# Optimization experiments

Measured on AMD Instinct MI355X. Metric: run time of the kernel, lower is better.

## Reference

```python
import jax, jax.numpy as jnp
import numpy as np

N = 50000   # nodes
E = 640000  # edges per outer layer
D = 128     # in_channels == num_hidden_channels
H = 4       # attention heads
C = D // H  # per-head dim = 32
BS = 1024   # batch_size for output slice
LN_EPS = 1e-12


def setup_inputs() -> dict:
    key = jax.random.key(0)
    ks = jax.random.split(key, 16)
    w = lambda k, shape: (jax.random.normal(k, shape, dtype=jnp.float32) * 0.05)
    return {
        "embs": jax.random.normal(ks[0], (N, D), dtype=jnp.float32),
        # GATv2 conv 0 (shared lin_l == lin_r since share_weights=True)
        "w0": w(ks[1], (D, H * C)),
        "b0": w(ks[2], (H * C,)),
        "att0": w(ks[3], (H, C)),
        "bias0": w(ks[4], (H * C,)),
        # GATv2 conv 1
        "w1": w(ks[5], (D, H * C)),
        "b1": w(ks[6], (H * C,)),
        "att1": w(ks[7], (H, C)),
        "bias1": w(ks[8], (H * C,)),
        # output head: Linear(D, D) + LayerNorm(D)
        "wout": w(ks[9], (D, D)),
        "bout": w(ks[10], (D,)),
        "gamma": jnp.ones((D,), dtype=jnp.float32),
        "beta": jnp.zeros((D,), dtype=jnp.float32),
        # graph structure (row 0 = source j, row 1 = target i, PyG convention)
        "edge_index0": jax.random.randint(ks[11], (2, E), 0, N, dtype=jnp.int32),
        "edge_index1": jax.random.randint(ks[12], (2, E), 0, N, dtype=jnp.int32),
        "batch_size": BS,
    }


def gatv2_conv(x, edge_index, w, b, att, bias):
    """PyG GATv2Conv: share_weights=True, add_self_loops=False, concat=True,
    negative_slope=0.2, edge_attr=None, eval mode (no attention dropout)."""
    xl = (x @ w + b).reshape(-1, H, C)          # [N, H, C]; x_l == x_r
    src, dst = edge_index[0], edge_index[1]
    xj = xl[src]                                # messages  [E, H, C]
    e = jax.nn.leaky_relu(xl[dst] + xj, negative_slope=0.2)
    alpha = jnp.einsum("ehc,hc->eh", e, att)    # [E, H]
    # segment softmax over incoming edges of each target node
    amax = jax.ops.segment_max(alpha, dst, num_segments=N)
    alpha = jnp.exp(alpha - amax[dst])
    denom = jax.ops.segment_sum(alpha, dst, num_segments=N)
    alpha = alpha / denom[dst]
    out = jax.ops.segment_sum(alpha[:, :, None] * xj, dst, num_segments=N)
    return out.reshape(-1, H * C) + bias        # [N, H*C]


def reference(embs, w0, b0, att0, bias0, w1, b1, att1, bias1,
              wout, bout, gamma, beta, edge_index0, edge_index1, batch_size):
    x = gatv2_conv(embs, edge_index0, w0, b0, att0, bias0)
    x = jax.nn.gelu(x, approximate=False)       # nn.GELU default (dropout is eval no-op)
    x = gatv2_conv(x, edge_index1, w1, b1, att1, bias1)
    # layernorm_output head on first batch_size nodes
    y = x[:batch_size] @ wout + bout
    mu = jnp.mean(y, axis=-1, keepdims=True)
    var = jnp.mean(jnp.square(y - mu), axis=-1, keepdims=True)
    return (y - mu) * jax.lax.rsqrt(var + LN_EPS) * gamma + beta
```

## Files before the change

kernel.cpp:

```cpp
#include <hip/hip_runtime.h>
#include <math.h>

#define DD 128
#define SLOT 64

typedef short bf16x8 __attribute__((ext_vector_type(8)));
typedef float f32x4  __attribute__((ext_vector_type(4)));

__device__ __forceinline__ unsigned bf16rne(float f) {
    unsigned u = __float_as_uint(f);
    return (u + 0x7FFFu + ((u >> 16) & 1u)) >> 16;
}
__device__ __forceinline__ float2 bf2f(unsigned u) {
    float2 r;
    r.x = __uint_as_float(u << 16);
    r.y = __uint_as_float(u & 0xFFFF0000u);
    return r;
}
__device__ __forceinline__ float gelu1(float v) {
    return 0.5f * v * (1.f + erff(v * 0.70710678118654752f));
}

__global__ __launch_bounds__(256) void k_zero(int* __restrict__ p, int T) {
    int stride = gridDim.x * 256;
    for (int i = blockIdx.x * 256 + threadIdx.x; i < T; i += stride) p[i] = 0;
}

__global__ __launch_bounds__(256) void k_mark(const int* __restrict__ src1,
                                              const int* __restrict__ dst1,
                                              int E1, int BS,
                                              unsigned* __restrict__ mb,
                                              int* __restrict__ livelist,
                                              int* __restrict__ nLive,
                                              int* __restrict__ cnt,
                                              int* __restrict__ ssrc, int N,
                                              const float* __restrict__ w0,
                                              const float* __restrict__ w1,
                                              unsigned short* __restrict__ wp0,
                                              unsigned short* __restrict__ wp1) {
    __shared__ int lbuf[1280];
    __shared__ int lcnt, lbase;
    if (threadIdx.x == 0) lcnt = 0;
    __syncthreads();

    int idx = blockIdx.x * 256 + threadIdx.x;
    if (idx < 2 * DD * DD) {
        const float* w = (idx < DD * DD) ? w0 : w1;
        unsigned short* wp = (idx < DD * DD) ? wp0 : wp1;
        int i = idx & (DD * DD - 1);
        int k = i >> 7, c = i & 127;
        int nt = c >> 4, ks = k >> 5;
        int lane = (c & 15) | (((k >> 3) & 3) << 4);
        wp[(((nt * 4 + ks) * 64) + lane) * 8 + (k & 7)] =
            (unsigned short)bf16rne(w[k * DD + c]);
    }

    int base = blockIdx.x * 1024 + threadIdx.x;
    #pragma unroll
    for (int j = 0; j < 4; ++j) {
        int e = base + j * 256;
        if (e < E1) {
            int d = dst1[e];
            if (d < BS) {
                int s = src1[e];
                int r = atomicAdd(&cnt[N + d], 1);
                if (r < SLOT) ssrc[(size_t)(N + d) * SLOT + r] = s;
                unsigned old = atomicOr(&mb[s >> 5], 1u << (s & 31));
                if (!((old >> (s & 31)) & 1u))
                    lbuf[atomicAdd(&lcnt, 1)] = s;
            }
        }
    }
    int g = blockIdx.x * 256 + threadIdx.x;
    if (g < BS) {
        unsigned old = atomicOr(&mb[g >> 5], 1u << (g & 31));
        if (!((old >> (g & 31)) & 1u))
            lbuf[atomicAdd(&lcnt, 1)] = g;
    }
    __syncthreads();
    if (threadIdx.x == 0) lbase = atomicAdd(nLive, lcnt);
    __syncthreads();
    for (int i = threadIdx.x; i < lcnt; i += 256) livelist[lbase + i] = lbuf[i];
}

__global__ __launch_bounds__(256) void k_hflin(
        const float* __restrict__ x, const unsigned short* __restrict__ wp,
        const float* __restrict__ b, unsigned* __restrict__ y, int nrows,
        int gLin,
        const int* __restrict__ src0, const int* __restrict__ dst0, int E0,
        const unsigned* __restrict__ mb, int* __restrict__ cnt,
        int* __restrict__ ssrc) {
    __shared__ bf16x8 wl[2048];

    if (blockIdx.x >= gLin) {
        int role = blockIdx.x - gLin;
        int base = role * 1024 + threadIdx.x;
        #pragma unroll
        for (int j = 0; j < 4; ++j) {
            int e = base + j * 256;
            if (e < E0) {
                int d = dst0[e];
                if ((mb[d >> 5] >> (d & 31)) & 1u) {
                    int r = atomicAdd(&cnt[d], 1);
                    if (r < SLOT) ssrc[(size_t)d * SLOT + r] = src0[e];
                }
            }
        }
        return;
    }

    const bf16x8* wg = (const bf16x8*)wp;
    #pragma unroll
    for (int i = 0; i < 8; ++i)
        wl[threadIdx.x + i * 256] = wg[threadIdx.x + i * 256];
    __syncthreads();

    int wave = threadIdx.x >> 6;
    int rb = blockIdx.x * 64 + wave * 16;
    int lane = threadIdx.x & 63;
    int c = lane & 15, g = lane >> 4;
    int rIn = rb + c;
    int rowValid = rIn < nrows;

    f32x4 acc[8];
    #pragma unroll
    for (int nt = 0; nt < 8; ++nt) {
        float bb = b[nt * 16 + c];
        acc[nt] = (f32x4){bb, bb, bb, bb};
    }
    for (int ks = 0; ks < 4; ++ks) {
        float xr[8];
        if (rowValid) {
            const float4* xp = (const float4*)&x[(size_t)rIn * DD + ks * 32 + g * 8];
            *(float4*)&xr[0] = xp[0];
            *(float4*)&xr[4] = xp[1];
        } else {
            #pragma unroll
            for (int j = 0; j < 8; ++j) xr[j] = 0.f;
        }
        union { unsigned u[4]; bf16x8 v; } af;
        #pragma unroll
        for (int j = 0; j < 4; ++j)
            af.u[j] = bf16rne(xr[2 * j]) | (bf16rne(xr[2 * j + 1]) << 16);
        #pragma unroll
        for (int nt = 0; nt < 8; ++nt) {
            bf16x8 bv = wl[(nt * 4 + ks) * 64 + lane];
            acc[nt] = __builtin_amdgcn_mfma_f32_16x16x32_bf16(af.v, bv, acc[nt], 0, 0, 0);
        }
    }
    int g4 = g * 4;
    #pragma unroll
    for (int nt = 0; nt < 8; ++nt) {
        #pragma unroll
        for (int reg = 0; reg < 4; ++reg) {
            unsigned u = bf16rne(acc[nt][reg]);
            unsigned up = (unsigned)__shfl_xor((int)u, 1, 64);
            int row = rb + g4 + reg;
            if (!(c & 1) && row < nrows)
                y[(size_t)row * 64 + (nt * 16 + c) / 2] = u | (up << 16);
        }
    }
}

__global__ __launch_bounds__(256) void k_aggL(const unsigned* __restrict__ xl,
                                              const int* __restrict__ cnt,
                                              const int* __restrict__ ssrc,
                                              const float* __restrict__ att,
                                              const float* __restrict__ bias,
                                              float* __restrict__ out,
                                              const int* __restrict__ livelist,
                                              const int* __restrict__ nLive) {
    int li = blockIdx.x * 4 + (threadIdx.x >> 6);
    if (li >= *nLive) return;
    int node = __builtin_amdgcn_readfirstlane(livelist[li]);
    int lane = threadIdx.x & 63;
    float2 attv = *(const float2*)&att[lane * 2];
    float2 xd = bf2f(xl[(size_t)node * 64 + lane]);
    int rs  = node * SLOT;
    int deg = cnt[node];
    deg = deg > SLOT ? SLOT : deg;

    float m = -3.4e38f, den = 0.f, accx = 0.f, accy = 0.f;
    int sA = (deg > 0) ? ssrc[rs] : 0;
    int sB = (deg > 1) ? ssrc[rs + 1] : 0;
    unsigned uA = xl[(size_t)sA * 64 + lane];
    unsigned uB = xl[(size_t)sB * 64 + lane];

    int k = 0;
    for (; k + 1 < deg; k += 2) {
        int sC = (k + 2 < deg) ? ssrc[rs + k + 2] : 0;
        int sD = (k + 3 < deg) ? ssrc[rs + k + 3] : 0;
        unsigned uC = xl[(size_t)sC * 64 + lane];
        unsigned uD = xl[(size_t)sD * 64 + lane];
        float2 vA = bf2f(uA), vB = bf2f(uB);

        float tx = xd.x + vA.x, ty = xd.y + vA.y;
        tx = tx > 0.f ? tx : 0.2f * tx;
        ty = ty > 0.f ? ty : 0.2f * ty;
        float l0 = tx * attv.x + ty * attv.y;
        tx = xd.x + vB.x; ty = xd.y + vB.y;
        tx = tx > 0.f ? tx : 0.2f * tx;
        ty = ty > 0.f ? ty : 0.2f * ty;
        float l1 = tx * attv.x + ty * attv.y;
        #pragma unroll
        for (int o = 8; o; o >>= 1) {
            l0 += __shfl_xor(l0, o, 64);
            l1 += __shfl_xor(l1, o, 64);
        }
        float mn = fmaxf(fmaxf(m, l0), l1);
        float corr = __expf(m - mn);
        float w0 = __expf(l0 - mn);
        float w1 = __expf(l1 - mn);
        den  = den  * corr + w0 + w1;
        accx = accx * corr + w0 * vA.x + w1 * vB.x;
        accy = accy * corr + w0 * vA.y + w1 * vB.y;
        m = mn;
        sA = sC; sB = sD; uA = uC; uB = uD;
    }
    if (k < deg) {
        float2 vA = bf2f(uA);
        float tx = xd.x + vA.x, ty = xd.y + vA.y;
        tx = tx > 0.f ? tx : 0.2f * tx;
        ty = ty > 0.f ? ty : 0.2f * ty;
        float l0 = tx * attv.x + ty * attv.y;
        #pragma unroll
        for (int o = 8; o; o >>= 1) l0 += __shfl_xor(l0, o, 64);
        float mn = fmaxf(m, l0);
        float corr = __expf(m - mn);
        float w0 = __expf(l0 - mn);
        den  = den  * corr + w0;
        accx = accx * corr + w0 * vA.x;
        accy = accy * corr + w0 * vA.y;
    }

    float inv = (deg > 0) ? 1.f / den : 0.f;
    float2 o2;
    o2.x = accx * inv + bias[lane * 2];
    o2.y = accy * inv + bias[lane * 2 + 1];
    *(float2*)&out[(size_t)node * DD + lane * 2] = o2;
}

__global__ __launch_bounds__(256) void k_linC(const float* __restrict__ x,
                                              const unsigned short* __restrict__ wp,
                                              const float* __restrict__ b,
                                              unsigned* __restrict__ y,
                                              const int* __restrict__ livelist,
                                              const int* __restrict__ nLive) {
    __shared__ bf16x8 wl[2048];
    int nL = *nLive;
    if (blockIdx.x * 64 >= nL) return;

    const bf16x8* wg = (const bf16x8*)wp;
    #pragma unroll
    for (int i = 0; i < 8; ++i)
        wl[threadIdx.x + i * 256] = wg[threadIdx.x + i * 256];
    __syncthreads();

    int wave = threadIdx.x >> 6;
    int lb = blockIdx.x * 64 + wave * 16;
    int lane = threadIdx.x & 63;
    int c = lane & 15, g = lane >> 4;
    int liIn = lb + c;
    int rIn = (liIn < nL) ? livelist[liIn] : 0;

    f32x4 acc[8];
    #pragma unroll
    for (int nt = 0; nt < 8; ++nt) {
        float bb = b[nt * 16 + c];
        acc[nt] = (f32x4){bb, bb, bb, bb};
    }
    for (int ks = 0; ks < 4; ++ks) {
        float xr[8];
        if (liIn < nL) {
            const float4* xp = (const float4*)&x[(size_t)rIn * DD + ks * 32 + g * 8];
            *(float4*)&xr[0] = xp[0];
            *(float4*)&xr[4] = xp[1];
            #pragma unroll
            for (int j = 0; j < 8; ++j) xr[j] = gelu1(xr[j]);
        } else {
            #pragma unroll
            for (int j = 0; j < 8; ++j) xr[j] = 0.f;
        }
        union { unsigned u[4]; bf16x8 v; } af;
        #pragma unroll
        for (int j = 0; j < 4; ++j)
            af.u[j] = bf16rne(xr[2 * j]) | (bf16rne(xr[2 * j + 1]) << 16);
        #pragma unroll
        for (int nt = 0; nt < 8; ++nt) {
            bf16x8 bv = wl[(nt * 4 + ks) * 64 + lane];
            acc[nt] = __builtin_amdgcn_mfma_f32_16x16x32_bf16(af.v, bv, acc[nt], 0, 0, 0);
        }
    }
    int g4 = g * 4;
    #pragma unroll
    for (int reg = 0; reg < 4; ++reg) {
        int liOut = lb + g4 + reg;
        int row = (liOut < nL) ? livelist[liOut] : -1;
        #pragma unroll
        for (int nt = 0; nt < 8; ++nt) {
            unsigned u = bf16rne(acc[nt][reg]);
            unsigned up = (unsigned)__shfl_xor((int)u, 1, 64);
            if (!(c & 1) && row >= 0)
                y[(size_t)row * 64 + (nt * 16 + c) / 2] = u | (up << 16);
        }
    }
}

__global__ __launch_bounds__(256) void k_agg1head(
        const unsigned* __restrict__ xl,
        const int* __restrict__ cnt, const int* __restrict__ ssrc,
        const float* __restrict__ att, const float* __restrict__ bias,
        const float* __restrict__ wout, const float* __restrict__ bout,
        const float* __restrict__ gamma, const float* __restrict__ beta,
        float* __restrict__ yout, int N, int BS) {
    __shared__ float xrow[4][DD];
    int wid  = threadIdx.x >> 6;
    int lane = threadIdx.x & 63;
    int node = blockIdx.x * 4 + wid;
    if (node >= BS) return;
    float2 attv = *(const float2*)&att[lane * 2];
    float2 xd = bf2f(xl[(size_t)node * 64 + lane]);
    int key = N + node;
    int rs  = key * SLOT;
    int deg = cnt[key];
    deg = deg > SLOT ? SLOT : deg;

    float m = -3.4e38f, den = 0.f, accx = 0.f, accy = 0.f;
    int sA = (deg > 0) ? ssrc[rs] : 0;
    int sB = (deg > 1) ? ssrc[rs + 1] : 0;
    unsigned uA = xl[(size_t)sA * 64 + lane];
    unsigned uB = xl[(size_t)sB * 64 + lane];

    int k = 0;
    for (; k + 1 < deg; k += 2) {
        int sC = (k + 2 < deg) ? ssrc[rs + k + 2] : 0;
        int sD = (k + 3 < deg) ? ssrc[rs + k + 3] : 0;
        unsigned uC = xl[(size_t)sC * 64 + lane];
        unsigned uD = xl[(size_t)sD * 64 + lane];
        float2 vA = bf2f(uA), vB = bf2f(uB);
        float tx = xd.x + vA.x, ty = xd.y + vA.y;
        tx = tx > 0.f ? tx : 0.2f * tx;
        ty = ty > 0.f ? ty : 0.2f * ty;
        float l0 = tx * attv.x + ty * attv.y;
        tx = xd.x + vB.x; ty = xd.y + vB.y;
        tx = tx > 0.f ? tx : 0.2f * tx;
        ty = ty > 0.f ? ty : 0.2f * ty;
        float l1 = tx * attv.x + ty * attv.y;
        #pragma unroll
        for (int o = 8; o; o >>= 1) {
            l0 += __shfl_xor(l0, o, 64);
            l1 += __shfl_xor(l1, o, 64);
        }
        float mn = fmaxf(fmaxf(m, l0), l1);
        float corr = __expf(m - mn);
        float w0 = __expf(l0 - mn);
        float w1 = __expf(l1 - mn);
        den  = den  * corr + w0 + w1;
        accx = accx * corr + w0 * vA.x + w1 * vB.x;
        accy = accy * corr + w0 * vA.y + w1 * vB.y;
        m = mn;
        sA = sC; sB = sD; uA = uC; uB = uD;
    }
    if (k < deg) {
        float2 vA = bf2f(uA);
        float tx = xd.x + vA.x, ty = xd.y + vA.y;
        tx = tx > 0.f ? tx : 0.2f * tx;
        ty = ty > 0.f ? ty : 0.2f * ty;
        float l0 = tx * attv.x + ty * attv.y;
        #pragma unroll
        for (int o = 8; o; o >>= 1) l0 += __shfl_xor(l0, o, 64);
        float mn = fmaxf(m, l0);
        float corr = __expf(m - mn);
        float w0 = __expf(l0 - mn);
        den  = den  * corr + w0;
        accx = accx * corr + w0 * vA.x;
        accy = accy * corr + w0 * vA.y;
    }

    float inv = (deg > 0) ? 1.f / den : 0.f;
    float2 o2;
    o2.x = accx * inv + bias[lane * 2];
    o2.y = accy * inv + bias[lane * 2 + 1];

    xrow[wid][lane * 2]     = o2.x;
    xrow[wid][lane * 2 + 1] = o2.y;
    float2 acc2 = *(const float2*)&bout[lane * 2];
    __syncthreads();
    #pragma unroll 4
    for (int kk = 0; kk < DD; ++kk) {
        float xv = xrow[wid][kk];
        float2 wv2 = *(const float2*)&wout[(size_t)kk * DD + lane * 2];
        acc2.x += xv * wv2.x;
        acc2.y += xv * wv2.y;
    }
    float s = acc2.x + acc2.y;
    #pragma unroll
    for (int o = 32; o; o >>= 1) s += __shfl_xor(s, o, 64);
    float mean = s * (1.f / 128.f);
    float dx = acc2.x - mean, dy = acc2.y - mean;
    float s2 = dx * dx + dy * dy;
    #pragma unroll
    for (int o = 32; o; o >>= 1) s2 += __shfl_xor(s2, o, 64);
    float rstd = rsqrtf(s2 * (1.f / 128.f) + 1e-12f);
    float2 g2 = *(const float2*)&gamma[lane * 2];
    float2 b2 = *(const float2*)&beta[lane * 2];
    float2 yo;
    yo.x = dx * rstd * g2.x + b2.x;
    yo.y = dy * rstd * g2.y + b2.y;
    *(float2*)&yout[(size_t)node * DD + lane * 2] = yo;
}

extern "C" void kernel_launch(void* const* d_in, const int* in_sizes, int n_in,
                              void* d_out, int out_size, void* d_ws, size_t ws_size,
                              hipStream_t stream) {
    const float* embs  = (const float*)d_in[0];
    const float* w0    = (const float*)d_in[1];
    const float* b0    = (const float*)d_in[2];
    const float* att0  = (const float*)d_in[3];
    const float* bias0 = (const float*)d_in[4];
    const float* w1    = (const float*)d_in[5];
    const float* b1    = (const float*)d_in[6];
    const float* att1  = (const float*)d_in[7];
    const float* bias1 = (const float*)d_in[8];
    const float* wout  = (const float*)d_in[9];
    const float* bout  = (const float*)d_in[10];
    const float* gamma = (const float*)d_in[11];
    const float* beta  = (const float*)d_in[12];
    const int* ei0 = (const int*)d_in[13];
    const int* ei1 = (const int*)d_in[14];

    int N  = in_sizes[0] / DD;
    int E0 = in_sizes[13] / 2;
    int E1 = in_sizes[14] / 2;
    int BS = out_size / DD;
    int n2 = N + BS;
    int W  = (N + 31) / 32;

    unsigned* xl   = (unsigned*)d_ws;
    float* out     = (float*)(xl + (size_t)N * 64);
    int* ssrc      = (int*)(out + (size_t)N * DD);
    int* cnt       = ssrc + (size_t)n2 * SLOT;
    unsigned* mb   = (unsigned*)(cnt + n2);
    int* nLive     = (int*)(mb + W + 32);
    int* livelist  = nLive + 1;
    unsigned short* wp0 = (unsigned short*)
        (((uintptr_t)(livelist + N) + 15) & ~(uintptr_t)15);
    unsigned short* wp1 = wp0 + DD * DD;

    int gH0  = (E0 + 1023) / 1024;
    int gH1  = (E1 + 1023) / 1024;
    int gLin = (N + 63) / 64;
    int Tz   = n2 + W + 32 + 1;

    k_zero<<<64, 256, 0, stream>>>(cnt, Tz);
    k_mark<<<gH1, 256, 0, stream>>>(ei1, ei1 + E1, E1, BS, mb, livelist, nLive,
                                    cnt, ssrc, N, w0, w1, wp0, wp1);
    k_hflin<<<gLin + gH0, 256, 0, stream>>>(
        embs, wp0, b0, xl, N, gLin, ei0, ei0 + E0, E0, mb, cnt, ssrc);
    k_aggL<<<(N + 3) / 4, 256, 0, stream>>>(xl, cnt, ssrc, att0, bias0, out,
                                            livelist, nLive);
    k_linC<<<gLin, 256, 0, stream>>>(out, wp1, b1, xl, livelist, nLive);
    k_agg1head<<<(BS + 3) / 4, 256, 0, stream>>>(
        xl, cnt, ssrc, att1, bias1,
        wout, bout, gamma, beta, (float*)d_out, N, BS);
}
```

Measured before the change: 79.74 us.

## Fuse GELU and bf16 packing into layer-0 aggregation; overlap count zeroing with marking

The layer-0 aggregation now applies bias, GELU and bf16 packing before storing, so the intermediate buffer shrinks from fp32 to packed bf16. The second linear kernel then loads bf16 fragments directly and drops its GELU and conversion work. Zeroing of the first-layer count array moves into extra blocks of the marking kernel, leaving a much smaller standalone zero kernel. The risk is a race: those zeroing blocks run concurrently with marking, which only touches the cnt[N+d] half, so this looks safe but depends on block ordering for nothing else.

```diff
diff --git a/kernel.cpp b/kernel.cpp
--- a/kernel.cpp
+++ b/kernel.cpp
@@ -21,7 +21,7 @@
     return 0.5f * v * (1.f + erff(v * 0.70710678118654752f));
 }
 
-__global__ __launch_bounds__(256) void k_zero(int* __restrict__ p, int T) {
+__global__ __launch_bounds__(256) void k_zero2(int* __restrict__ p, int T) {
     int stride = gridDim.x * 256;
     for (int i = blockIdx.x * 256 + threadIdx.x; i < T; i += stride) p[i] = 0;
 }
@@ -37,13 +37,21 @@
                                               const float* __restrict__ w0,
                                               const float* __restrict__ w1,
                                               unsigned short* __restrict__ wp0,
-                                              unsigned short* __restrict__ wp1) {
+                                              unsigned short* __restrict__ wp1,
+                                              int gZ) {
+    if (blockIdx.x < gZ) {
+        int stride = gZ * 256;
+        for (int i = blockIdx.x * 256 + threadIdx.x; i < N; i += stride)
+            cnt[i] = 0;
+        return;
+    }
     __shared__ int lbuf[1280];
     __shared__ int lcnt, lbase;
     if (threadIdx.x == 0) lcnt = 0;
     __syncthreads();
 
-    int idx = blockIdx.x * 256 + threadIdx.x;
+    int role = blockIdx.x - gZ;
+    int idx = role * 256 + threadIdx.x;
     if (idx < 2 * DD * DD) {
         const float* w = (idx < DD * DD) ? w0 : w1;
         unsigned short* wp = (idx < DD * DD) ? wp0 : wp1;
@@ -55,7 +63,7 @@
             (unsigned short)bf16rne(w[k * DD + c]);
     }
 
-    int base = blockIdx.x * 1024 + threadIdx.x;
+    int base = role * 1024 + threadIdx.x;
     #pragma unroll
     for (int j = 0; j < 4; ++j) {
         int e = base + j * 256;
@@ -71,7 +79,7 @@
             }
         }
     }
-    int g = blockIdx.x * 256 + threadIdx.x;
+    int g = role * 256 + threadIdx.x;
     if (g < BS) {
         unsigned old = atomicOr(&mb[g >> 5], 1u << (g & 31));
         if (!((old >> (g & 31)) & 1u))
@@ -143,10 +151,9 @@
         for (int j = 0; j < 4; ++j)
             af.u[j] = bf16rne(xr[2 * j]) | (bf16rne(xr[2 * j + 1]) << 16);
         #pragma unroll
-        for (int nt = 0; nt < 8; ++nt) {
-            bf16x8 bv = wl[(nt * 4 + ks) * 64 + lane];
-            acc[nt] = __builtin_amdgcn_mfma_f32_16x16x32_bf16(af.v, bv, acc[nt], 0, 0, 0);
-        }
+        for (int nt = 0; nt < 8; ++nt)
+            acc[nt] = __builtin_amdgcn_mfma_f32_16x16x32_bf16(
+                af.v, wl[(nt * 4 + ks) * 64 + lane], acc[nt], 0, 0, 0);
     }
     int g4 = g * 4;
     #pragma unroll
@@ -167,7 +174,7 @@
                                               const int* __restrict__ ssrc,
                                               const float* __restrict__ att,
                                               const float* __restrict__ bias,
-                                              float* __restrict__ out,
+                                              unsigned* __restrict__ xg,
                                               const int* __restrict__ livelist,
                                               const int* __restrict__ nLive) {
     int li = blockIdx.x * 4 + (threadIdx.x >> 6);
@@ -234,13 +241,12 @@
     }
 
     float inv = (deg > 0) ? 1.f / den : 0.f;
-    float2 o2;
-    o2.x = accx * inv + bias[lane * 2];
-    o2.y = accy * inv + bias[lane * 2 + 1];
-    *(float2*)&out[(size_t)node * DD + lane * 2] = o2;
-}
-
-__global__ __launch_bounds__(256) void k_linC(const float* __restrict__ x,
+    float gx = gelu1(accx * inv + bias[lane * 2]);
+    float gy = gelu1(accy * inv + bias[lane * 2 + 1]);
+    xg[(size_t)node * 64 + lane] = bf16rne(gx) | (bf16rne(gy) << 16);
+}
+
+__global__ __launch_bounds__(256) void k_linC(const unsigned* __restrict__ xg,
                                               const unsigned short* __restrict__ wp,
                                               const float* __restrict__ b,
                                               unsigned* __restrict__ y,
@@ -262,6 +268,7 @@
     int c = lane & 15, g = lane >> 4;
     int liIn = lb + c;
     int rIn = (liIn < nL) ? livelist[liIn] : 0;
+    const uint4* xp = (const uint4*)&xg[(size_t)rIn * 64];
 
     f32x4 acc[8];
     #pragma unroll
@@ -269,27 +276,15 @@
         float bb = b[nt * 16 + c];
         acc[nt] = (f32x4){bb, bb, bb, bb};
     }
+    #pragma unroll
     for (int ks = 0; ks < 4; ++ks) {
-        float xr[8];
-        if (liIn < nL) {
-            const float4* xp = (const float4*)&x[(size_t)rIn * DD + ks * 32 + g * 8];
-            *(float4*)&xr[0] = xp[0];
-            *(float4*)&xr[4] = xp[1];
-            #pragma unroll
-            for (int j = 0; j < 8; ++j) xr[j] = gelu1(xr[j]);
-        } else {
-            #pragma unroll
-            for (int j = 0; j < 8; ++j) xr[j] = 0.f;
-        }
-        union { unsigned u[4]; bf16x8 v; } af;
-        #pragma unroll
-        for (int j = 0; j < 4; ++j)
-            af.u[j] = bf16rne(xr[2 * j]) | (bf16rne(xr[2 * j + 1]) << 16);
-        #pragma unroll
-        for (int nt = 0; nt < 8; ++nt) {
-            bf16x8 bv = wl[(nt * 4 + ks) * 64 + lane];
-            acc[nt] = __builtin_amdgcn_mfma_f32_16x16x32_bf16(af.v, bv, acc[nt], 0, 0, 0);
-        }
+        union { uint4 q; bf16x8 v; } af;
+        if (liIn < nL) af.q = xp[ks * 4 + g];
+        else           af.q = make_uint4(0, 0, 0, 0);
+        #pragma unroll
+        for (int nt = 0; nt < 8; ++nt)
+            acc[nt] = __builtin_amdgcn_mfma_f32_16x16x32_bf16(
+                af.v, wl[(nt * 4 + ks) * 64 + lane], acc[nt], 0, 0, 0);
     }
     int g4 = g * 4;
     #pragma unroll
@@ -437,8 +432,8 @@
     int W  = (N + 31) / 32;
 
     unsigned* xl   = (unsigned*)d_ws;
-    float* out     = (float*)(xl + (size_t)N * 64);
-    int* ssrc      = (int*)(out + (size_t)N * DD);
+    unsigned* xg   = xl + (size_t)N * 64;
+    int* ssrc      = (int*)(xg + (size_t)N * 64);
     int* cnt       = ssrc + (size_t)n2 * SLOT;
     unsigned* mb   = (unsigned*)(cnt + n2);
     int* nLive     = (int*)(mb + W + 32);
@@ -450,16 +445,18 @@
     int gH0  = (E0 + 1023) / 1024;
     int gH1  = (E1 + 1023) / 1024;
     int gLin = (N + 63) / 64;
-    int Tz   = n2 + W + 32 + 1;
-
-    k_zero<<<64, 256, 0, stream>>>(cnt, Tz);
-    k_mark<<<gH1, 256, 0, stream>>>(ei1, ei1 + E1, E1, BS, mb, livelist, nLive,
-                                    cnt, ssrc, N, w0, w1, wp0, wp1);
+    int gZ   = 48;
+    int Tz2  = BS + W + 32 + 1;
+
+    k_zero2<<<4, 256, 0, stream>>>(cnt + N, Tz2);
+    k_mark<<<gZ + gH1, 256, 0, stream>>>(ei1, ei1 + E1, E1, BS, mb, livelist,
+                                         nLive, cnt, ssrc, N, w0, w1, wp0, wp1,
+                                         gZ);
     k_hflin<<<gLin + gH0, 256, 0, stream>>>(
         embs, wp0, b0, xl, N, gLin, ei0, ei0 + E0, E0, mb, cnt, ssrc);
-    k_aggL<<<(N + 3) / 4, 256, 0, stream>>>(xl, cnt, ssrc, att0, bias0, out,
+    k_aggL<<<(N + 3) / 4, 256, 0, stream>>>(xl, cnt, ssrc, att0, bias0, xg,
                                             livelist, nLive);
-    k_linC<<<gLin, 256, 0, stream>>>(out, wp1, b1, xl, livelist, nLive);
+    k_linC<<<gLin, 256, 0, stream>>>(xg, wp1, b1, xl, livelist, nLive);
     k_agg1head<<<(BS + 3) / 4, 256, 0, stream>>>(
         xl, cnt, ssrc, att1, bias1,
         wout, bout, gamma, beta, (float*)d_out, N, BS);
```

Result: faster. 77.84 us (-2.4%).
